# Optimization experiments

Measured on AMD Instinct MI355X. Metric: run time of the kernel, lower is better.

## Reference

```python
import jax, jax.numpy as jnp
import numpy as np

N_ROW, N_COL, RANK = 8192, 8192, 256

def setup_inputs() -> dict:
    key = jax.random.key(0)
    k1, k2, k3 = jax.random.split(key, 3)
    X = jax.random.normal(k1, (N_ROW, RANK), dtype=jnp.float32)
    Y = jax.random.normal(k2, (RANK, N_COL), dtype=jnp.float32)
    beta = jax.random.normal(k3, (1,), dtype=jnp.float32)
    return {"X": X, "Y": Y, "beta": beta}

def reference(X, Y, beta):
    # mathematically equal to torch.norm(X[:,None] - Y.T, dim=-1).
    x2 = jnp.sum(X * X, axis=1, keepdims=True)          # (n_row, 1)
    y2 = jnp.sum(Y * Y, axis=0, keepdims=True)          # (1, n_col)
    cross = X @ Y                                        # (n_row, n_col) GEMM
    d2 = jnp.maximum(x2 + y2 - 2.0 * cross, 0.0)
    norms = jnp.sqrt(d2)
    z = -norms + beta                                    # beta broadcasts (1,)
    return z
```

## Files before the change

kernel.cpp:

```cpp
#include <hip/hip_runtime.h>

#define NROW 8192
#define NCOL 8192
#define RANK 256

#define BM 128
#define BN 128

typedef __bf16  bf16x8 __attribute__((ext_vector_type(8)));
typedef float   f32x4  __attribute__((ext_vector_type(4)));

__device__ __forceinline__ unsigned short f2bf(float f) {
    unsigned int u = __builtin_bit_cast(unsigned int, f);
    u += 0x7fffu + ((u >> 16) & 1u);
    return (unsigned short)(u >> 16);
}

__global__ __launch_bounds__(256) void prep_x(const float* __restrict__ X,
                                              unsigned short* __restrict__ Xb,
                                              float* __restrict__ x2) {
    const int row  = blockIdx.x * 4 + (threadIdx.x >> 6);
    const int lane = threadIdx.x & 63;
    const float4 v = ((const float4*)(X + (size_t)row * RANK))[lane];
    float s = v.x * v.x + v.y * v.y + v.z * v.z + v.w * v.w;
    ushort4 b;
    b.x = f2bf(v.x); b.y = f2bf(v.y); b.z = f2bf(v.z); b.w = f2bf(v.w);
    ((ushort4*)(Xb + (size_t)row * RANK))[lane] = b;
    #pragma unroll
    for (int off = 32; off > 0; off >>= 1) s += __shfl_down(s, off);
    if (lane == 0) x2[row] = s;
}

__global__ __launch_bounds__(256) void prep_y(const float* __restrict__ Y,
                                              unsigned short* __restrict__ Ybt,
                                              float* __restrict__ y2) {
    __shared__ float tile[64][65];
    __shared__ float part[256];
    const int t  = threadIdx.x;
    const int j0 = blockIdx.x * 64;
    const int tq = t >> 6;
    const int tl = t & 63;
    float acc = 0.f;
    for (int c = 0; c < 4; ++c) {
        const int k0 = c * 64;
        #pragma unroll
        for (int i = 0; i < 16; ++i) {
            const int kk = tq * 16 + i;
            const float v = Y[(size_t)(k0 + kk) * NCOL + j0 + tl];
            tile[kk][tl] = v;
            acc += v * v;
        }
        __syncthreads();
        #pragma unroll
        for (int i = 0; i < 16; ++i) {
            const int jj = tq * 16 + i;
            Ybt[(size_t)(j0 + jj) * RANK + k0 + tl] = f2bf(tile[tl][jj]);
        }
        __syncthreads();
    }
    part[t] = acc;
    __syncthreads();
    if (t < 64)
        y2[j0 + t] = part[t] + part[t + 64] + part[t + 128] + part[t + 192];
}

__global__ __launch_bounds__(256, 2)
void l2_gemm(const unsigned short* __restrict__ A,
             const unsigned short* __restrict__ Bt,
             const float* __restrict__ x2,
             const float* __restrict__ y2,
             const float* __restrict__ beta_p,
             float* __restrict__ out) {
    __shared__ alignas(16) unsigned short Bs[BN * RANK];

    const int t    = threadIdx.x;
    const int wid  = t >> 6;
    const int lane = t & 63;

    const int bid  = blockIdx.x;
    const int xcd  = bid & 7;
    const int seq  = bid >> 3;
    const int ct   = xcd * 8 + (seq & 7);
    const int rt   = seq >> 3;
    const int rowBase = rt * BM;
    const int colBase = ct * BN;

    const int waveM = (wid >> 1) * 64;
    const int waveN = (wid & 1) * 64;

    f32x4 acc[4][4] = {};

    {
        const int l5 = lane >> 5;
        const int ls = lane & 31;
        #pragma unroll
        for (int r = 0; r < 16; ++r) {
            const int ro = wid * 32 + r * 2 + l5;
            const int cs = ls ^ (ro & 7);
            const unsigned short* gp =
                Bt + (size_t)(colBase + ro) * RANK + cs * 8;
            unsigned short* lp = &Bs[(wid * 32 + r * 2) * RANK];
            __builtin_amdgcn_global_load_lds(
                (__attribute__((address_space(1))) void*)gp,
                (__attribute__((address_space(3))) void*)lp, 16, 0, 0);
        }
    }

    const int r0 = rowBase + waveM + (lane & 15);
    const int c0 = colBase + waveN + ((lane >> 4) << 2);
    const int koff = (lane >> 4) * 8;

    bf16x8 af0[4];
    #pragma unroll
    for (int mt = 0; mt < 4; ++mt)
        af0[mt] = *(const bf16x8*)(A + (size_t)(r0 + mt * 16) * RANK + koff);

    const float beta = *beta_p;
    float xv[4];
    f32x4 y4[4];
    #pragma unroll
    for (int mt = 0; mt < 4; ++mt) xv[mt] = x2[r0 + mt * 16];
    #pragma unroll
    for (int nt = 0; nt < 4; ++nt) y4[nt] = *(const f32x4*)(y2 + c0 + nt * 16);

    __syncthreads();

    #pragma unroll
    for (int kg = 0; kg < 8; ++kg) {
        bf16x8 af[4], bfr[4];
        if (kg == 0) {
            #pragma unroll
            for (int mt = 0; mt < 4; ++mt) af[mt] = af0[mt];
        } else {
            const int ko = kg * 32 + koff;
            #pragma unroll
            for (int mt = 0; mt < 4; ++mt)
                af[mt] = *(const bf16x8*)(A + (size_t)(r0 + mt * 16) * RANK + ko);
        }
        const int sbase = kg * 4 + (lane >> 4);
        #pragma unroll
        for (int nt = 0; nt < 4; ++nt) {
            const int rr = waveN + nt * 16 + (lane & 15);
            const int s  = sbase ^ (rr & 7);
            bfr[nt] = *(const bf16x8*)(&Bs[rr * RANK + s * 8]);
        }
        #pragma unroll
        for (int mt = 0; mt < 4; ++mt)
            #pragma unroll
            for (int nt = 0; nt < 4; ++nt)
                acc[mt][nt] = __builtin_amdgcn_mfma_f32_16x16x32_bf16(
                    bfr[nt], af[mt], acc[mt][nt], 0, 0, 0);
    }

    #pragma unroll
    for (int mt = 0; mt < 4; ++mt) {
        const int row = r0 + mt * 16;
        float* op = out + (size_t)row * NCOL + c0;
        #pragma unroll
        for (int nt = 0; nt < 4; ++nt) {
            const f32x4 a = acc[mt][nt];
            f32x4 z;
            #pragma unroll
            for (int r = 0; r < 4; ++r) {
                float d2 = xv[mt] + y4[nt][r] - 2.0f * a[r];
                z[r] = beta - __builtin_amdgcn_sqrtf(fmaxf(d2, 0.0f));
            }
            __builtin_nontemporal_store(z, (f32x4*)(op + nt * 16));
        }
    }
}

extern "C" void kernel_launch(void* const* d_in, const int* in_sizes, int n_in,
                              void* d_out, int out_size, void* d_ws, size_t ws_size,
                              hipStream_t stream) {
    const float* X    = (const float*)d_in[0];
    const float* Y    = (const float*)d_in[1];
    const float* beta = (const float*)d_in[2];
    float* out = (float*)d_out;

    char* ws = (char*)d_ws;
    unsigned short* Xb  = (unsigned short*)(ws);
    unsigned short* Ybt = (unsigned short*)(ws + (size_t)4 * 1024 * 1024);
    float* x2 = (float*)(ws + (size_t)8 * 1024 * 1024);
    float* y2 = (float*)(ws + (size_t)8 * 1024 * 1024 + 32 * 1024);

    prep_x<<<NROW / 4, 256, 0, stream>>>(X, Xb, x2);
    prep_y<<<NCOL / 64, 256, 0, stream>>>(Y, Ybt, y2);

    l2_gemm<<<dim3(4096), 256, 0, stream>>>(Xb, Ybt, x2, y2, beta, out);
}
```

Before: 350.9 us.

## Make GEMM blocks persistent over row tiles, reusing the LDS-resident B column slab

Each block now loads one 128-column slab of transposed Y into LDS once and then loops over 8 consecutive row tiles, computing and storing each 128x128 output tile in turn. The grid shrinks from 4096 to 512 blocks. The goal is to cut the repeated B loads into LDS and the per-block launch overhead. In exchange there is less parallelism, since 512 blocks on 256 CUs gives about two per CU. The serial row loop also has no overlap between A loads and the epilogue stores, and the wave-to-quadrant mapping is swapped.

```diff
diff --git a/kernel.cpp b/kernel.cpp
--- a/kernel.cpp
+++ b/kernel.cpp
@@ -6,6 +6,7 @@
 
 #define BM 128
 #define BN 128
+#define NRT 8
 
 typedef __bf16  bf16x8 __attribute__((ext_vector_type(8)));
 typedef float   f32x4  __attribute__((ext_vector_type(4)));
@@ -77,18 +78,11 @@
     const int wid  = t >> 6;
     const int lane = t & 63;
 
-    const int bid  = blockIdx.x;
-    const int xcd  = bid & 7;
-    const int seq  = bid >> 3;
-    const int ct   = xcd * 8 + (seq & 7);
-    const int rt   = seq >> 3;
-    const int rowBase = rt * BM;
-    const int colBase = ct * BN;
-
-    const int waveM = (wid >> 1) * 64;
-    const int waveN = (wid & 1) * 64;
-
-    f32x4 acc[4][4] = {};
+    const int b   = blockIdx.x;
+    const int cs  = b >> 3;
+    const int rg  = b & 7;
+    const int colBase    = cs * BN;
+    const int rowGrpBase = rg * (NRT * BM);
 
     {
         const int l5 = lane >> 5;
@@ -96,9 +90,9 @@
         #pragma unroll
         for (int r = 0; r < 16; ++r) {
             const int ro = wid * 32 + r * 2 + l5;
-            const int cs = ls ^ (ro & 7);
+            const int cslot = ls ^ (ro & 7);
             const unsigned short* gp =
-                Bt + (size_t)(colBase + ro) * RANK + cs * 8;
+                Bt + (size_t)(colBase + ro) * RANK + cslot * 8;
             unsigned short* lp = &Bs[(wid * 32 + r * 2) * RANK];
             __builtin_amdgcn_global_load_lds(
                 (__attribute__((address_space(1))) void*)gp,
@@ -106,66 +100,65 @@
         }
     }
 
-    const int r0 = rowBase + waveM + (lane & 15);
-    const int c0 = colBase + waveN + ((lane >> 4) << 2);
-    const int koff = (lane >> 4) * 8;
-
-    bf16x8 af0[4];
-    #pragma unroll
-    for (int mt = 0; mt < 4; ++mt)
-        af0[mt] = *(const bf16x8*)(A + (size_t)(r0 + mt * 16) * RANK + koff);
+    const int waveM = (wid & 1) * 64;
+    const int waveN = (wid >> 1) * 64;
+    const int koff  = (lane >> 4) * 8;
+    const int c0    = colBase + waveN + ((lane >> 4) << 2);
 
     const float beta = *beta_p;
-    float xv[4];
     f32x4 y4[4];
-    #pragma unroll
-    for (int mt = 0; mt < 4; ++mt) xv[mt] = x2[r0 + mt * 16];
     #pragma unroll
     for (int nt = 0; nt < 4; ++nt) y4[nt] = *(const f32x4*)(y2 + c0 + nt * 16);
 
     __syncthreads();
 
-    #pragma unroll
-    for (int kg = 0; kg < 8; ++kg) {
-        bf16x8 af[4], bfr[4];
-        if (kg == 0) {
-            #pragma unroll
-            for (int mt = 0; mt < 4; ++mt) af[mt] = af0[mt];
-        } else {
+    #pragma unroll 1
+    for (int rt = 0; rt < NRT; ++rt) {
+        const int rowBase = rowGrpBase + rt * BM;
+        const int r0 = rowBase + waveM + (lane & 15);
+
+        float xv[4];
+        #pragma unroll
+        for (int mt = 0; mt < 4; ++mt) xv[mt] = x2[r0 + mt * 16];
+
+        f32x4 acc[4][4] = {};
+        #pragma unroll
+        for (int kg = 0; kg < 8; ++kg) {
+            bf16x8 af[4], bfr[4];
             const int ko = kg * 32 + koff;
             #pragma unroll
             for (int mt = 0; mt < 4; ++mt)
                 af[mt] = *(const bf16x8*)(A + (size_t)(r0 + mt * 16) * RANK + ko);
+            const int sbase = kg * 4 + (lane >> 4);
+            #pragma unroll
+            for (int nt = 0; nt < 4; ++nt) {
+                const int rr = waveN + nt * 16 + (lane & 15);
+                const int s  = sbase ^ (rr & 7);
+                bfr[nt] = *(const bf16x8*)(&Bs[rr * RANK + s * 8]);
+            }
+            #pragma unroll
+            for (int mt = 0; mt < 4; ++mt)
+                #pragma unroll
+                for (int nt = 0; nt < 4; ++nt)
+                    acc[mt][nt] = __builtin_amdgcn_mfma_f32_16x16x32_bf16(
+                        bfr[nt], af[mt], acc[mt][nt], 0, 0, 0);
         }
-        const int sbase = kg * 4 + (lane >> 4);
+
         #pragma unroll
-        for (int nt = 0; nt < 4; ++nt) {
-            const int rr = waveN + nt * 16 + (lane & 15);
-            const int s  = sbase ^ (rr & 7);
-            bfr[nt] = *(const bf16x8*)(&Bs[rr * RANK + s * 8]);
-        }
-        #pragma unroll
-        for (int mt = 0; mt < 4; ++mt)
+        for (int mt = 0; mt < 4; ++mt) {
+            const int row = r0 + mt * 16;
+            float* op = out + (size_t)row * NCOL + c0;
             #pragma unroll
-            for (int nt = 0; nt < 4; ++nt)
-                acc[mt][nt] = __builtin_amdgcn_mfma_f32_16x16x32_bf16(
-                    bfr[nt], af[mt], acc[mt][nt], 0, 0, 0);
-    }
-
-    #pragma unroll
-    for (int mt = 0; mt < 4; ++mt) {
-        const int row = r0 + mt * 16;
-        float* op = out + (size_t)row * NCOL + c0;
-        #pragma unroll
-        for (int nt = 0; nt < 4; ++nt) {
-            const f32x4 a = acc[mt][nt];
-            f32x4 z;
-            #pragma unroll
-            for (int r = 0; r < 4; ++r) {
-                float d2 = xv[mt] + y4[nt][r] - 2.0f * a[r];
-                z[r] = beta - __builtin_amdgcn_sqrtf(fmaxf(d2, 0.0f));
+            for (int nt = 0; nt < 4; ++nt) {
+                const f32x4 a = acc[mt][nt];
+                f32x4 z;
+                #pragma unroll
+                for (int r = 0; r < 4; ++r) {
+                    float d2 = xv[mt] + y4[nt][r] - 2.0f * a[r];
+                    z[r] = beta - __builtin_amdgcn_sqrtf(fmaxf(d2, 0.0f));
+                }
+                __builtin_nontemporal_store(z, (f32x4*)(op + nt * 16));
             }
-            __builtin_nontemporal_store(z, (f32x4*)(op + nt * 16));
         }
     }
 }
@@ -187,5 +180,5 @@
     prep_x<<<NROW / 4, 256, 0, stream>>>(X, Xb, x2);
     prep_y<<<NCOL / 64, 256, 0, stream>>>(Y, Ybt, y2);
 
-    l2_gemm<<<dim3(4096), 256, 0, stream>>>(Xb, Ybt, x2, y2, beta, out);
+    l2_gemm<<<dim3(512), 256, 0, stream>>>(Xb, Ybt, x2, y2, beta, out);
 }
```

Result: faster. 341.6 us (-2.6%).
